# Kernel tuning notes

Measured on AMD Instinct MI355X. Metric: run time of the kernel, lower is better.

## Reference

```python
import jax, jax.numpy as jnp
import numpy as np

BZ, NF, D = 8, 10000, 16
H = W = 512


def setup_inputs() -> dict:
    key = jax.random.key(0)
    k1, k2, k3 = jax.random.split(key, 3)
    attrs = jax.random.normal(k1, (BZ, NF, 3, D), dtype=jnp.float32)
    # barycentric weights: positive, sum to 1 over the 3 vertices
    u = jax.random.uniform(k2, (BZ, H, W, 3), dtype=jnp.float32, minval=1e-3, maxval=1.0)
    baryw_buffer = u / jnp.sum(u, axis=-1, keepdims=True)
    # triangle indices into the flattened [BZ*NF] face table; -1 = empty pixel
    triangle_buffer = jax.random.randint(k3, (BZ, H, W), -1, BZ * NF, dtype=jnp.int32)
    return {"attrs": attrs, "baryw_buffer": baryw_buffer, "triangle_buffer": triangle_buffer}


def reference(attrs, baryw_buffer, triangle_buffer):
    # attrs: [N, NF, 3, D]; baryw_buffer: [N, H, W, 3]; triangle_buffer: [N, H, W] int (-1 = bg)
    N, H_, W_ = triangle_buffer.shape
    Dd = attrs.shape[-1]
    flat_attrs = attrs.reshape(-1, 3, Dd)                      # [N*NF, 3, D]
    mask = triangle_buffer == -1                               # [N, H, W]
    idx = jnp.where(mask, 0, triangle_buffer)                  # clamp bg to 0
    pixel_face_vals = flat_attrs[idx]                          # [N, H, W, 3, D] gather
    pixel_vals = jnp.einsum('nhwk,nhwkd->nhwd', baryw_buffer, pixel_face_vals)
    pixel_vals = jnp.where(mask[..., None], 0.0, pixel_vals)   # zero background
    out = jnp.moveaxis(pixel_vals, -1, 1)                      # [N, D, H, W]
    vis = (~mask).astype(jnp.float32)[:, None]                 # [N, 1, H, W]
    return jnp.concatenate([out, vis], axis=1)                 # [N, D+1, H, W]
```

## Files before the change

### kernel.cpp

```cpp
#include <hip/hip_runtime.h>
#include <hip/hip_fp16.h>

constexpr int BZ = 8, NF = 10000, D = 16, HImg = 512, WImg = 512;
constexpr int HW = HImg * WImg;
constexpr int NPIX = BZ * HW;
constexpr int NFACES = BZ * NF;
constexpr int PIX_PER_THREAD = 4;
constexpr int NTHREADS = NPIX / PIX_PER_THREAD;
constexpr int BLOCK = 256;
constexpr size_t REC_USHORTS = 64;
constexpr size_t WS_NEEDED = (size_t)NFACES * 128;

constexpr int NPHASE = 4;
constexpr int FACES_PER_PHASE = NFACES / NPHASE;

typedef float f32x4 __attribute__((ext_vector_type(4)));
typedef int   i32x4 __attribute__((ext_vector_type(4)));

__global__ __launch_bounds__(BLOCK) void convert_kernel(
    const float* __restrict__ attrs, ushort* __restrict__ rec)
{
    const int tid = blockIdx.x * BLOCK + threadIdx.x;
    if (tid >= NFACES * 6) return;
    const int face = tid / 6;
    const int c    = tid - face * 6;
    const float4* src = reinterpret_cast<const float4*>(
        attrs + (size_t)face * 48 + c * 8);
    const float4 a = src[0], b = src[1];
    __half h[8];
    h[0] = __float2half_rn(a.x); h[1] = __float2half_rn(a.y);
    h[2] = __float2half_rn(a.z); h[3] = __float2half_rn(a.w);
    h[4] = __float2half_rn(b.x); h[5] = __float2half_rn(b.y);
    h[6] = __float2half_rn(b.z); h[7] = __float2half_rn(b.w);
    *reinterpret_cast<int4*>(rec + (size_t)face * REC_USHORTS + c * 8) =
        *reinterpret_cast<const int4*>(h);
}

__device__ inline void h8_to_f8(int4 raw, float f[8]) {
    const __half2* hp = reinterpret_cast<const __half2*>(&raw);
#pragma unroll
    for (int q = 0; q < 4; ++q) {
        const float2 t = __half22float2(hp[q]);
        f[2 * q]     = t.x;
        f[2 * q + 1] = t.y;
    }
}

__global__ __launch_bounds__(BLOCK, 4) void render_f16_sweep_kernel(
    const ushort* __restrict__ rec,
    const float*  __restrict__ baryw,
    const int*    __restrict__ tri,
    float*        __restrict__ out)
{
    const int tid = blockIdx.x * BLOCK + threadIdx.x;
    const int p0  = tid * PIX_PER_THREAD;

    const int n   = p0 / HW;
    const int pix = p0 - n * HW;

    const i32x4 t4 = __builtin_nontemporal_load(
        reinterpret_cast<const i32x4*>(tri + p0));
    const f32x4* bw = reinterpret_cast<const f32x4*>(baryw + (size_t)p0 * 3);
    const f32x4 b0 = __builtin_nontemporal_load(bw + 0);
    const f32x4 b1 = __builtin_nontemporal_load(bw + 1);
    const f32x4 b2 = __builtin_nontemporal_load(bw + 2);

    float w[PIX_PER_THREAD][3] = {
        {b0.x, b0.y, b0.z},
        {b0.w, b1.x, b1.y},
        {b1.z, b1.w, b2.x},
        {b2.y, b2.z, b2.w},
    };
    const int t[PIX_PER_THREAD] = {t4.x, t4.y, t4.z, t4.w};

    float vis[PIX_PER_THREAD];
#pragma unroll
    for (int j = 0; j < PIX_PER_THREAD; ++j) {
        const bool bg = (t[j] < 0);
        vis[j] = bg ? 0.0f : 1.0f;
        w[j][0] *= vis[j];
        w[j][1] *= vis[j];
        w[j][2] *= vis[j];
    }

    const int4* rec4 = reinterpret_cast<const int4*>(rec);

    float r[PIX_PER_THREAD][D];
#pragma unroll
    for (int j = 0; j < PIX_PER_THREAD; ++j)
#pragma unroll
        for (int i = 0; i < D; ++i) r[j][i] = 0.0f;

#pragma unroll
    for (int ph = 0; ph < NPHASE; ++ph) {
        const int lo = ph * FACES_PER_PHASE;
#pragma unroll
        for (int j = 0; j < PIX_PER_THREAD; ++j) {
            if ((unsigned)(t[j] - lo) < (unsigned)FACES_PER_PHASE) {
                const int4* rb = rec4 + (size_t)t[j] * 8;
                const int4 V0 = rb[0];
                const int4 V1 = rb[1];
                const int4 V2 = rb[2];
                const int4 V3 = rb[3];
                const int4 V4 = rb[4];
                const int4 V5 = rb[5];
                float a0[8], a1[8], a2[8], a3[8], a4[8], a5[8];
                h8_to_f8(V0, a0); h8_to_f8(V1, a1);
                h8_to_f8(V2, a2); h8_to_f8(V3, a3);
                h8_to_f8(V4, a4); h8_to_f8(V5, a5);
#pragma unroll
                for (int i = 0; i < 8; ++i) {
                    r[j][i]     += w[j][0] * a0[i] + w[j][1] * a2[i]
                                 + w[j][2] * a4[i];
                    r[j][8 + i] += w[j][0] * a1[i] + w[j][1] * a3[i]
                                 + w[j][2] * a5[i];
                }
            }
        }
        if (ph != NPHASE - 1) __syncthreads();
    }

    const size_t outbase = (size_t)n * (D + 1) * HW + pix;
#pragma unroll
    for (int d = 0; d < D; ++d) {
        f32x4 o;
        o.x = r[0][d]; o.y = r[1][d]; o.z = r[2][d]; o.w = r[3][d];
        __builtin_nontemporal_store(
            o, reinterpret_cast<f32x4*>(out + outbase + (size_t)d * HW));
    }
    f32x4 v;
    v.x = vis[0]; v.y = vis[1]; v.z = vis[2]; v.w = vis[3];
    __builtin_nontemporal_store(
        v, reinterpret_cast<f32x4*>(out + outbase + (size_t)D * HW));
}

__global__ __launch_bounds__(BLOCK) void renderer_f32_kernel(
    const float* __restrict__ attrs,
    const float* __restrict__ baryw,
    const int*   __restrict__ tri,
    float*       __restrict__ out)
{
    const int tid = blockIdx.x * BLOCK + threadIdx.x;
    const int p0  = tid * PIX_PER_THREAD;
    if (p0 >= NPIX) return;

    const int n   = p0 / HW;
    const int pix = p0 - n * HW;

    const int4 t4 = *reinterpret_cast<const int4*>(tri + p0);
    const float4* bw = reinterpret_cast<const float4*>(baryw + (size_t)p0 * 3);
    const float4 b0 = bw[0], b1 = bw[1], b2 = bw[2];

    float w[PIX_PER_THREAD][3] = {
        {b0.x, b0.y, b0.z},
        {b0.w, b1.x, b1.y},
        {b1.z, b1.w, b2.x},
        {b2.y, b2.z, b2.w},
    };
    const int t[PIX_PER_THREAD] = {t4.x, t4.y, t4.z, t4.w};

    float vis[PIX_PER_THREAD];
    const float4* abase[PIX_PER_THREAD];
#pragma unroll
    for (int j = 0; j < PIX_PER_THREAD; ++j) {
        const bool bg = (t[j] < 0);
        vis[j] = bg ? 0.0f : 1.0f;
        const int tc = bg ? 0 : t[j];
        abase[j] = reinterpret_cast<const float4*>(attrs + (size_t)tc * (3 * D));
        w[j][0] *= vis[j];
        w[j][1] *= vis[j];
        w[j][2] *= vis[j];
    }

    const size_t outbase = (size_t)n * (D + 1) * HW + pix;

#pragma unroll
    for (int c = 0; c < 4; ++c) {
        float r[PIX_PER_THREAD][4];
#pragma unroll
        for (int j = 0; j < PIX_PER_THREAD; ++j) {
            const float4 a0 = abase[j][c];
            const float4 a1 = abase[j][4 + c];
            const float4 a2 = abase[j][8 + c];
            r[j][0] = w[j][0] * a0.x + w[j][1] * a1.x + w[j][2] * a2.x;
            r[j][1] = w[j][0] * a0.y + w[j][1] * a1.y + w[j][2] * a2.y;
            r[j][2] = w[j][0] * a0.z + w[j][1] * a1.z + w[j][2] * a2.z;
            r[j][3] = w[j][0] * a0.w + w[j][1] * a1.w + w[j][2] * a2.w;
        }
#pragma unroll
        for (int i = 0; i < 4; ++i) {
            const int d = c * 4 + i;
            float4 o;
            o.x = r[0][i]; o.y = r[1][i]; o.z = r[2][i]; o.w = r[3][i];
            *reinterpret_cast<float4*>(out + outbase + (size_t)d * HW) = o;
        }
    }

    float4 v;
    v.x = vis[0]; v.y = vis[1]; v.z = vis[2]; v.w = vis[3];
    *reinterpret_cast<float4*>(out + outbase + (size_t)D * HW) = v;
}

extern "C" void kernel_launch(void* const* d_in, const int* in_sizes, int n_in,
                              void* d_out, int out_size, void* d_ws, size_t ws_size,
                              hipStream_t stream) {
    const float* attrs = (const float*)d_in[0];
    const float* baryw = (const float*)d_in[1];
    const int*   tri   = (const int*)d_in[2];
    float*       out   = (float*)d_out;

    const int grid = NTHREADS / BLOCK;

    if (ws_size >= WS_NEEDED) {
        ushort* rec = (ushort*)d_ws;
        const int conv_grid = (NFACES * 6 + BLOCK - 1) / BLOCK;
        convert_kernel<<<conv_grid, BLOCK, 0, stream>>>(attrs, rec);
        render_f16_sweep_kernel<<<grid, BLOCK, 0, stream>>>(rec, baryw, tri, out);
    } else {
        renderer_f32_kernel<<<grid, BLOCK, 0, stream>>>(attrs, baryw, tri, out);
    }
}
```

Measured before the change: 208.6 us.

## Cooperatively stage gathered face records through swizzled LDS per phase

Replaces each thread's own six 16-byte gathers of a face record with a cooperative scheme. Groups of 8 lanes fetch one record's 8 int4 segments, so each global gather is a contiguous 128-byte read. The records go into XOR-swizzled shared memory, and each thread then reads its own record back from LDS. This adds about 32 block barriers per thread, 32KB+ of shared memory that may limit occupancy, and also loads the two unused padding segments.

```diff
diff --git a/kernel.cpp b/kernel.cpp
--- a/kernel.cpp
+++ b/kernel.cpp
@@ -46,14 +46,18 @@
     }
 }
 
-__global__ __launch_bounds__(BLOCK, 4) void render_f16_sweep_kernel(
+__global__ __launch_bounds__(BLOCK, 4) void render_coop_kernel(
     const ushort* __restrict__ rec,
     const float*  __restrict__ baryw,
     const int*    __restrict__ tri,
     float*        __restrict__ out)
 {
-    const int tid = blockIdx.x * BLOCK + threadIdx.x;
-    const int p0  = tid * PIX_PER_THREAD;
+    __shared__ int  s_face[BLOCK * PIX_PER_THREAD];
+    __shared__ int4 s_rec[BLOCK * 8];
+
+    const int tidx = threadIdx.x;
+    const int tid  = blockIdx.x * BLOCK + tidx;
+    const int p0   = tid * PIX_PER_THREAD;
 
     const int n   = p0 / HW;
     const int pix = p0 - n * HW;
@@ -81,7 +85,9 @@
         w[j][0] *= vis[j];
         w[j][1] *= vis[j];
         w[j][2] *= vis[j];
-    }
+        s_face[tidx * PIX_PER_THREAD + j] = t[j];
+    }
+    __syncthreads();
 
     const int4* rec4 = reinterpret_cast<const int4*>(rec);
 
@@ -91,33 +97,47 @@
 #pragma unroll
         for (int i = 0; i < D; ++i) r[j][i] = 0.0f;
 
-#pragma unroll
+    const int krec = tidx >> 3;
+    const int seg  = tidx & 7;
+
     for (int ph = 0; ph < NPHASE; ++ph) {
         const int lo = ph * FACES_PER_PHASE;
 #pragma unroll
         for (int j = 0; j < PIX_PER_THREAD; ++j) {
-            if ((unsigned)(t[j] - lo) < (unsigned)FACES_PER_PHASE) {
-                const int4* rb = rec4 + (size_t)t[j] * 8;
-                const int4 V0 = rb[0];
-                const int4 V1 = rb[1];
-                const int4 V2 = rb[2];
-                const int4 V3 = rb[3];
-                const int4 V4 = rb[4];
-                const int4 V5 = rb[5];
-                float a0[8], a1[8], a2[8], a3[8], a4[8], a5[8];
-                h8_to_f8(V0, a0); h8_to_f8(V1, a1);
-                h8_to_f8(V2, a2); h8_to_f8(V3, a3);
-                h8_to_f8(V4, a4); h8_to_f8(V5, a5);
-#pragma unroll
-                for (int i = 0; i < 8; ++i) {
-                    r[j][i]     += w[j][0] * a0[i] + w[j][1] * a2[i]
-                                 + w[j][2] * a4[i];
-                    r[j][8 + i] += w[j][0] * a1[i] + w[j][1] * a3[i]
-                                 + w[j][2] * a5[i];
+#pragma unroll
+            for (int pass = 0; pass < 8; ++pass) {
+                const int slot = pass * 32 + krec;
+                const int f = s_face[slot * PIX_PER_THREAD + j];
+                if ((unsigned)(f - lo) < (unsigned)FACES_PER_PHASE) {
+                    const int4 v = rec4[(size_t)f * 8 + seg];
+                    s_rec[slot * 8 + (seg ^ (slot & 7))] = v;
                 }
             }
+            __syncthreads();
+            if ((unsigned)(t[j] - lo) < (unsigned)FACES_PER_PHASE) {
+                const int sw = tidx & 7;
+                float a[8];
+                h8_to_f8(s_rec[tidx * 8 + (0 ^ sw)], a);
+#pragma unroll
+                for (int i = 0; i < 8; ++i) r[j][i]     += w[j][0] * a[i];
+                h8_to_f8(s_rec[tidx * 8 + (1 ^ sw)], a);
+#pragma unroll
+                for (int i = 0; i < 8; ++i) r[j][8 + i] += w[j][0] * a[i];
+                h8_to_f8(s_rec[tidx * 8 + (2 ^ sw)], a);
+#pragma unroll
+                for (int i = 0; i < 8; ++i) r[j][i]     += w[j][1] * a[i];
+                h8_to_f8(s_rec[tidx * 8 + (3 ^ sw)], a);
+#pragma unroll
+                for (int i = 0; i < 8; ++i) r[j][8 + i] += w[j][1] * a[i];
+                h8_to_f8(s_rec[tidx * 8 + (4 ^ sw)], a);
+#pragma unroll
+                for (int i = 0; i < 8; ++i) r[j][i]     += w[j][2] * a[i];
+                h8_to_f8(s_rec[tidx * 8 + (5 ^ sw)], a);
+#pragma unroll
+                for (int i = 0; i < 8; ++i) r[j][8 + i] += w[j][2] * a[i];
+            }
+            __syncthreads();
         }
-        if (ph != NPHASE - 1) __syncthreads();
     }
 
     const size_t outbase = (size_t)n * (D + 1) * HW + pix;
@@ -215,7 +235,7 @@
         ushort* rec = (ushort*)d_ws;
         const int conv_grid = (NFACES * 6 + BLOCK - 1) / BLOCK;
         convert_kernel<<<conv_grid, BLOCK, 0, stream>>>(attrs, rec);
-        render_f16_sweep_kernel<<<grid, BLOCK, 0, stream>>>(rec, baryw, tri, out);
+        render_coop_kernel<<<grid, BLOCK, 0, stream>>>(rec, baryw, tri, out);
     } else {
         renderer_f32_kernel<<<grid, BLOCK, 0, stream>>>(attrs, baryw, tri, out);
     }
```

New measurement: 295.7 us. +41.8%, slower.
